# Performance work log

Measured on AMD Instinct MI355X. Metric: run time of the kernel, lower is better.

Reference implementation:

```python
import jax, jax.numpy as jnp
import numpy as np

D_MODEL = 512
NUM_HEADS = 8
D_FF = 2048
HEAD_DIM = D_MODEL // NUM_HEADS
EPS = 1e-8


def rmsnorm(x, scale):
    rms = jax.lax.rsqrt(jnp.mean(x * x, axis=-1, keepdims=True) + EPS)
    return scale * x * rms


def alibi_bias(seq_len, num_heads):
    # faithful to: 1.0 / (arange(1,H+1) * 2**arange(0,8)[:,None]).flatten()[:H]
    a = jnp.arange(1, num_heads + 1, dtype=jnp.float32)          # (H,)
    b = 2.0 ** jnp.arange(0, 8, dtype=jnp.float32)[:, None]       # (8,1)
    slopes = (1.0 / (a * b).reshape(-1))[:num_heads]               # (H,)
    pos = jnp.arange(seq_len)
    dist = jnp.abs(pos[:, None] - pos[None, :]).astype(jnp.float32)  # (S,S)
    return -slopes[:, None, None] * dist[None]                     # (H,S,S)


def setup_inputs() -> dict:
    key = jax.random.key(0)
    ks = jax.random.split(key, 12)
    s = 0.02
    return {
        "x": jax.random.normal(ks[0], (2, 2048, D_MODEL), dtype=jnp.float32),
        "norm1_scale": jnp.ones((D_MODEL,), jnp.float32),
        "norm2_scale": jnp.ones((D_MODEL,), jnp.float32),
        "in_proj_w": jax.random.normal(ks[1], (3 * D_MODEL, D_MODEL), jnp.float32) * s,
        "in_proj_b": jnp.zeros((3 * D_MODEL,), jnp.float32),
        "out_proj_w": jax.random.normal(ks[2], (D_MODEL, D_MODEL), jnp.float32) * s,
        "out_proj_b": jnp.zeros((D_MODEL,), jnp.float32),
        "w1": jax.random.normal(ks[3], (D_FF, D_MODEL), jnp.float32) * s,
        "b1": jnp.zeros((D_FF,), jnp.float32),
        "w2": jax.random.normal(ks[4], (D_MODEL, D_FF), jnp.float32) * s,
        "b2": jnp.zeros((D_MODEL,), jnp.float32),
    }


def reference(x, norm1_scale, norm2_scale, in_proj_w, in_proj_b,
              out_proj_w, out_proj_b, w1, b1, w2, b2):
    B, S, D = x.shape
    xn = rmsnorm(x, norm1_scale)
    qkv = xn @ in_proj_w.T + in_proj_b                      # (B,S,3D)
    q, k, v = jnp.split(qkv, 3, axis=-1)
    q = q.reshape(B, S, NUM_HEADS, HEAD_DIM)
    k = k.reshape(B, S, NUM_HEADS, HEAD_DIM)
    v = v.reshape(B, S, NUM_HEADS, HEAD_DIM)
    scale = 1.0 / jnp.sqrt(jnp.float32(HEAD_DIM))
    scores = jnp.einsum('bqhd,bkhd->bhqk', q, k) * scale    # (B,H,S,S)
    scores = scores + alibi_bias(S, NUM_HEADS)[None]
    attn = jax.nn.softmax(scores, axis=-1)
    ctx = jnp.einsum('bhqk,bkhd->bqhd', attn, v).reshape(B, S, D)
    attn_out = ctx @ out_proj_w.T + out_proj_b
    x = x + attn_out                                        # dropout is identity (eval)
    xn2 = rmsnorm(x, norm2_scale)
    h = jax.nn.gelu(xn2 @ w1.T + b1, approximate=False)
    mlp_out = h @ w2.T + b2
    return x + mlp_out
```

## Files before the change

kernel.cpp:

```cpp
#include <hip/hip_runtime.h>
#include <math.h>


typedef __bf16 bf16x8 __attribute__((ext_vector_type(8)));
typedef float  f32x4  __attribute__((ext_vector_type(4)));

#define TOKENS 4096
#define DMODEL 512
#define SEQ    2048
#define QSCALE 0.1803368801f

__device__ __forceinline__ void gl_lds16(const __bf16* g, __bf16* l) {
    __builtin_amdgcn_global_load_lds(
        (const __attribute__((address_space(1))) void*)g,
        (__attribute__((address_space(3))) void*)l, 16, 0, 0);
}

union PkU { unsigned u; __bf16 h[2]; };

__global__ void pre_kernel(const float* __restrict__ x, const float* __restrict__ n1s,
                           __bf16* __restrict__ xn1,
                           const float* __restrict__ w0, const float* __restrict__ w1,
                           const float* __restrict__ w2, const float* __restrict__ w3,
                           __bf16* __restrict__ d0, __bf16* __restrict__ d1,
                           __bf16* __restrict__ d2, __bf16* __restrict__ d3) {
    if (blockIdx.x < 1024) {
        int wave = threadIdx.x >> 6, lane = threadIdx.x & 63;
        int tok = blockIdx.x * 4 + wave;
        const float* row = x + (size_t)tok * DMODEL;
        float4 v0 = *(const float4*)&row[lane * 4];
        float4 v1 = *(const float4*)&row[256 + lane * 4];
        float ss = v0.x*v0.x + v0.y*v0.y + v0.z*v0.z + v0.w*v0.w
                 + v1.x*v1.x + v1.y*v1.y + v1.z*v1.z + v1.w*v1.w;
        #pragma unroll
        for (int off = 1; off < 64; off <<= 1) ss += __shfl_xor(ss, off);
        float r = rsqrtf(ss * (1.0f / DMODEL) + 1e-8f);
        __bf16* o = xn1 + (size_t)tok * DMODEL;
        o[lane*4 + 0] = (__bf16)(v0.x * r * n1s[lane*4 + 0]);
        o[lane*4 + 1] = (__bf16)(v0.y * r * n1s[lane*4 + 1]);
        o[lane*4 + 2] = (__bf16)(v0.z * r * n1s[lane*4 + 2]);
        o[lane*4 + 3] = (__bf16)(v0.w * r * n1s[lane*4 + 3]);
        o[256 + lane*4 + 0] = (__bf16)(v1.x * r * n1s[256 + lane*4 + 0]);
        o[256 + lane*4 + 1] = (__bf16)(v1.y * r * n1s[256 + lane*4 + 1]);
        o[256 + lane*4 + 2] = (__bf16)(v1.z * r * n1s[256 + lane*4 + 2]);
        o[256 + lane*4 + 3] = (__bf16)(v1.w * r * n1s[256 + lane*4 + 3]);
    } else {
        const int N0 = 1536 * 512, N1 = 512 * 512, N2 = 2048 * 512, N3 = 512 * 2048;
        int i4 = ((blockIdx.x - 1024) * 256 + threadIdx.x) * 4;
        const float* s; __bf16* d;
        if (i4 < N0)              { s = w0 + i4;  d = d0 + i4; }
        else if ((i4 -= N0) < N1) { s = w1 + i4;  d = d1 + i4; }
        else if ((i4 -= N1) < N2) { s = w2 + i4;  d = d2 + i4; }
        else if ((i4 -= N2) < N3) { s = w3 + i4;  d = d3 + i4; }
        else return;
        float4 v = *(const float4*)s;
        d[0] = (__bf16)v.x; d[1] = (__bf16)v.y; d[2] = (__bf16)v.z; d[3] = (__bf16)v.w;
    }
}

__global__ void rmsnorm_kernel(const float* __restrict__ x, const float* __restrict__ scale,
                               __bf16* __restrict__ out) {
    int wave = threadIdx.x >> 6, lane = threadIdx.x & 63;
    int tok = blockIdx.x * 4 + wave;
    const float* row = x + (size_t)tok * DMODEL;
    float4 v0 = *(const float4*)&row[lane * 4];
    float4 v1 = *(const float4*)&row[256 + lane * 4];
    float ss = v0.x*v0.x + v0.y*v0.y + v0.z*v0.z + v0.w*v0.w
             + v1.x*v1.x + v1.y*v1.y + v1.z*v1.z + v1.w*v1.w;
    #pragma unroll
    for (int off = 1; off < 64; off <<= 1) ss += __shfl_xor(ss, off);
    float r = rsqrtf(ss * (1.0f / DMODEL) + 1e-8f);
    __bf16* o = out + (size_t)tok * DMODEL;
    o[lane*4 + 0] = (__bf16)(v0.x * r * scale[lane*4 + 0]);
    o[lane*4 + 1] = (__bf16)(v0.y * r * scale[lane*4 + 1]);
    o[lane*4 + 2] = (__bf16)(v0.z * r * scale[lane*4 + 2]);
    o[lane*4 + 3] = (__bf16)(v0.w * r * scale[lane*4 + 3]);
    o[256 + lane*4 + 0] = (__bf16)(v1.x * r * scale[256 + lane*4 + 0]);
    o[256 + lane*4 + 1] = (__bf16)(v1.y * r * scale[256 + lane*4 + 1]);
    o[256 + lane*4 + 2] = (__bf16)(v1.z * r * scale[256 + lane*4 + 2]);
    o[256 + lane*4 + 3] = (__bf16)(v1.w * r * scale[256 + lane*4 + 3]);
}

template <int EPI, int TM, int KS = 1>
__global__ __launch_bounds__(256) void gemm_bt(
    const __bf16* __restrict__ A, const __bf16* __restrict__ W,
    const float* __restrict__ bias, const float* __restrict__ res,
    float* __restrict__ Cf, __bf16* __restrict__ Cb,
    __bf16* __restrict__ qb, __bf16* __restrict__ kb, __bf16* __restrict__ vtb,
    int M, int N, int K)
{
    constexpr int RI = TM / 32;
    __shared__ alignas(16) __bf16 As[2][TM * 32];
    __shared__ alignas(16) __bf16 Bs[2][128 * 32];
    const int tid = threadIdx.x;
    const int bm = blockIdx.x * TM;
    const int bn = blockIdx.y * 128;
    const int wave = tid >> 6, lane = tid & 63;
    const int wm = (wave & 1) * (TM / 2), wn = (wave >> 1) * 64;
    const int lrow = lane & 15;
    const int kq = (lane >> 4) * 8;

    f32x4 acc[RI][4] = {};

    const int Kc = K / KS;
    const int kbeg = (KS > 1) ? blockIdx.z * Kc : 0;

    for (int k0 = kbeg; k0 < kbeg + Kc; k0 += 64) {
        __syncthreads();
        #pragma unroll
        for (int i = 0; i < TM / 32; i++) {
            int tt = i * 256 + tid;
            int kh = tt / (TM * 4), rem = tt % (TM * 4);
            int mrow = rem >> 2, c8 = rem & 3;
            gl_lds16(&A[(size_t)(bm + mrow) * K + k0 + kh * 32 + c8 * 8],
                     (__bf16*)As + tt * 8);
        }
        #pragma unroll
        for (int i = 0; i < 4; i++) {
            int tt = i * 256 + tid;
            int kh = tt >> 9, rem = tt & 511;
            int nrow = rem >> 2, c8 = rem & 3;
            gl_lds16(&W[(size_t)(bn + nrow) * K + k0 + kh * 32 + c8 * 8],
                     (__bf16*)Bs + tt * 8);
        }
        __syncthreads();
        #pragma unroll
        for (int kh = 0; kh < 2; kh++) {
            bf16x8 af[RI], bfv[4];
            #pragma unroll
            for (int i = 0; i < RI; i++) af[i] = *(bf16x8*)&As[kh][(wm + i*16 + lrow)*32 + kq];
            #pragma unroll
            for (int j = 0; j < 4; j++) bfv[j] = *(bf16x8*)&Bs[kh][(wn + j*16 + lrow)*32 + kq];
            #pragma unroll
            for (int i = 0; i < RI; i++)
                #pragma unroll
                for (int j = 0; j < 4; j++)
                    acc[i][j] = __builtin_amdgcn_mfma_f32_16x16x32_bf16(af[i], bfv[j], acc[i][j], 0, 0, 0);
        }
    }

    const int crow0 = (lane >> 4) * 4;
    const int ccol = lane & 15;
    const int quad = lane >> 4;

    if (EPI == 4) {
        #pragma unroll
        for (int j = 0; j < 4; j++) {
            const int col = bn + wn + j * 16 + ccol;
            const float bv = bias[col];
            if (col < 512) {
                const int h = col >> 6, d = col & 63;
                #pragma unroll
                for (int i = 0; i < RI; i++) {
                    const int row0 = bm + wm + i * 16 + crow0;
                    const int b = row0 >> 11, s0 = row0 & 2047;
                    #pragma unroll
                    for (int r = 0; r < 4; r++)
                        qb[(((size_t)b*8 + h)*2048 + s0 + r)*64 + d] =
                            (__bf16)((acc[i][j][r] + bv) * QSCALE);
                }
            } else if (col < 1024) {
                const int h = (col - 512) >> 6, d = col & 63;
                #pragma unroll
                for (int i = 0; i < RI; i++) {
                    const int row0 = bm + wm + i * 16 + crow0;
                    const int b = row0 >> 11, s0 = row0 & 2047;
                    #pragma unroll
                    for (int r = 0; r < 4; r++)
                        kb[(((size_t)b*8 + h)*2048 + s0 + r)*64 + d] = (__bf16)(acc[i][j][r] + bv);
                }
            } else {
                const int h = (col - 1024) >> 6, d = col & 63;
                const int tok0 = bm + wm;
                const int b = tok0 >> 11, sbase = tok0 & 2047;
                unsigned* vrow = (unsigned*)vtb + (((size_t)b*8 + h)*64 + d) * 1024 + (sbase >> 1);
                #pragma unroll
                for (int ip = 0; ip < RI / 2; ip++) {
                    #pragma unroll
                    for (int r = 0; r < 4; r++) {
                        PkU pk;
                        pk.h[0] = (__bf16)(acc[2*ip][j][r] + bv);
                        pk.h[1] = (__bf16)(acc[2*ip+1][j][r] + bv);
                        vrow[ip * 16 + quad * 4 + r] = pk.u;
                    }
                }
            }
        }
    } else {
        #pragma unroll
        for (int i = 0; i < RI; i++) {
            const int row0 = bm + wm + i * 16 + crow0;
            #pragma unroll
            for (int j = 0; j < 4; j++) {
                const int col = bn + wn + j * 16 + ccol;
                if (EPI == 1) {
                    const float bv = bias[col];
                    #pragma unroll
                    for (int r = 0; r < 4; r++) {
                        const size_t idx = (size_t)(row0 + r) * N + col;
                        Cf[idx] = res[idx] + acc[i][j][r] + bv;
                    }
                } else if (EPI == 2) {
                    const float bv = bias[col];
                    #pragma unroll
                    for (int r = 0; r < 4; r++) {
                        float v = acc[i][j][r] + bv;
                        float u = v * (0.7978845608f + 0.0356774081f * v * v);
                        float t = exp2f(u * 2.8853900818f);
                        Cb[(size_t)(row0 + r) * N + col] = (__bf16)(v - v / (t + 1.0f));
                    }
                } else {
                    const size_t zoff = (size_t)blockIdx.z * M * N;
                    #pragma unroll
                    for (int r = 0; r < 4; r++)
                        Cf[zoff + (size_t)(row0 + r) * N + col] = acc[i][j][r];
                }
            }
        }
    }
}

__global__ __launch_bounds__(256) void attn_kernel(
    const __bf16* __restrict__ qb, const __bf16* __restrict__ kb,
    const __bf16* __restrict__ vtb, __bf16* __restrict__ ctx)
{
    const int id = blockIdx.x;
    const int qt = id >> 4;
    const int bh = (id & 15) ^ (7 * (id >> 8));
    const int h = bh & 7, b = bh >> 3;
    const int tid = threadIdx.x, wave = tid >> 6, lane = tid & 63;
    const int lrow = lane & 15, quad = lane >> 4;

    __shared__ alignas(16) __bf16 Ks[2][2][64 * 32];
    __shared__ alignas(16) __bf16 Vt[2][2][64 * 32];
    __shared__ alignas(16) unsigned Pt4[4][2][16][20];

    const float slope2 = -1.44269504f / (float)(h + 1);
    const int q0 = qt * 64;
    const int D = 16 * (h + 1) + 16;
    const int kt_lo = max(0, q0 - D) >> 6;
    const int kt_hi = min(SEQ - 1, q0 + 63 + D) >> 6;

    bf16x8 qf[2];
    #pragma unroll
    for (int dh = 0; dh < 2; dh++)
        qf[dh] = *(const bf16x8*)&qb[((size_t)bh*2048 + q0 + wave*16 + lrow)*64 + dh*32 + quad*8];

    bf16x8 ones;
    #pragma unroll
    for (int j = 0; j < 8; j++) ones[j] = (__bf16)1.0f;

    f32x4 O[4] = {};
    f32x4 lacc = {};

    auto stage = [&](int kt, int buf) {
        const int kbase = kt * 64;
        #pragma unroll
        for (int i = 0; i < 2; i++) {
            int tt = i * 256 + tid;
            int dh = tt >> 8, key = (tt & 255) >> 2, c8 = (tt & 3) * 8;
            gl_lds16(&kb[((size_t)bh*2048 + kbase + key)*64 + dh*32 + c8],
                     (__bf16*)Ks[buf] + tt * 8);
        }
        #pragma unroll
        for (int i = 0; i < 2; i++) {
            int tt = i * 256 + tid;
            int kh = tt >> 8, d = (tt & 255) >> 2, ck = (tt & 3) * 8;
            gl_lds16(&vtb[((size_t)bh*64 + d)*2048 + kbase + kh*32 + ck],
                     (__bf16*)Vt[buf] + tt * 8);
        }
    };

    stage(kt_lo, 0);

    for (int kt = kt_lo, buf = 0; kt <= kt_hi; kt++, buf ^= 1) {
        __syncthreads();
        if (kt < kt_hi) stage(kt + 1, buf ^ 1);

        bf16x8 kf[4][2];
        #pragma unroll
        for (int j = 0; j < 4; j++)
            #pragma unroll
            for (int dh = 0; dh < 2; dh++)
                kf[j][dh] = *(bf16x8*)&Ks[buf][dh][(j*16 + lrow)*32 + quad*8];

        f32x4 Sc[4] = {};
        #pragma unroll
        for (int dh = 0; dh < 2; dh++)
            #pragma unroll
            for (int j = 0; j < 4; j++)
                Sc[j] = __builtin_amdgcn_mfma_f32_16x16x32_bf16(qf[dh], kf[j][dh], Sc[j], 0, 0, 0);

        const float dbase = (float)(q0 + wave*16 + quad*4 - kt*64 - lrow);
        #pragma unroll
        for (int r = 0; r < 4; r++) {
            const float d0 = dbase + (float)r;
            #pragma unroll
            for (int jp = 0; jp < 2; jp++) {
                float v0 = fmaf(slope2, fabsf(d0 - (float)(jp*32)),      Sc[2*jp  ][r]);
                float v1 = fmaf(slope2, fabsf(d0 - (float)(jp*32 + 16)), Sc[2*jp+1][r]);
                PkU pk;
                pk.h[0] = (__bf16)exp2f(v0);
                pk.h[1] = (__bf16)exp2f(v1);
                Pt4[wave][jp][quad*4 + r][lrow] = pk.u;
            }
        }

        bf16x8 pf[2];
        #pragma unroll
        for (int kh = 0; kh < 2; kh++)
            pf[kh] = *(bf16x8*)&Pt4[wave][kh][lrow][quad*4];

        #pragma unroll
        for (int kh = 0; kh < 2; kh++)
            lacc = __builtin_amdgcn_mfma_f32_16x16x32_bf16(pf[kh], ones, lacc, 0, 0, 0);

        #pragma unroll
        for (int dt = 0; dt < 4; dt++) {
            #pragma unroll
            for (int kh = 0; kh < 2; kh++) {
                bf16x8 vf = *(bf16x8*)&Vt[buf][kh][(dt*16 + lrow)*32 + quad*8];
                O[dt] = __builtin_amdgcn_mfma_f32_16x16x32_bf16(pf[kh], vf, O[dt], 0, 0, 0);
            }
        }
    }

    #pragma unroll
    for (int dt = 0; dt < 4; dt++) {
        #pragma unroll
        for (int r = 0; r < 4; r++) {
            const int q = q0 + wave*16 + quad*4 + r;
            ctx[((size_t)(b * 2048 + q)) * DMODEL + h * 64 + dt*16 + lrow] =
                (__bf16)(O[dt][r] / lacc[r]);
        }
    }
}

__global__ void combine2_kernel(const float* __restrict__ p, const float* __restrict__ x1,
                                const float* __restrict__ b2, float* __restrict__ out) {
    const int i4 = (blockIdx.x * 256 + threadIdx.x) * 4;
    float4 a  = *(const float4*)&x1[i4];
    float4 b  = *(const float4*)&b2[i4 & 511];
    float4 c0 = *(const float4*)&p[i4];
    float4 c1 = *(const float4*)&p[(size_t)TOKENS * DMODEL + i4];
    float4 o;
    o.x = a.x + b.x + c0.x + c1.x;
    o.y = a.y + b.y + c0.y + c1.y;
    o.z = a.z + b.z + c0.z + c1.z;
    o.w = a.w + b.w + c0.w + c1.w;
    *(float4*)&out[i4] = o;
}

extern "C" void kernel_launch(void* const* d_in, const int* in_sizes, int n_in,
                              void* d_out, int out_size, void* d_ws, size_t ws_size,
                              hipStream_t stream) {
    const float* x    = (const float*)d_in[0];
    const float* n1s  = (const float*)d_in[1];
    const float* n2s  = (const float*)d_in[2];
    const float* wqkv = (const float*)d_in[3];
    const float* bqkv = (const float*)d_in[4];
    const float* wout = (const float*)d_in[5];
    const float* bout = (const float*)d_in[6];
    const float* w1   = (const float*)d_in[7];
    const float* b1   = (const float*)d_in[8];
    const float* w2   = (const float*)d_in[9];
    const float* b2   = (const float*)d_in[10];
    float* out = (float*)d_out;

    char* ws = (char*)d_ws;
    __bf16* xn1     = (__bf16*)ws; ws += (size_t)TOKENS * DMODEL * 2;
    __bf16* qbuf    = (__bf16*)ws; ws += (size_t)TOKENS * DMODEL * 2;
    __bf16* kbuf    = (__bf16*)ws; ws += (size_t)TOKENS * DMODEL * 2;
    __bf16* vtbuf   = (__bf16*)ws; ws += (size_t)TOKENS * DMODEL * 2;
    __bf16* wqkv_b  = (__bf16*)ws; ws += (size_t)1536 * DMODEL * 2;
    __bf16* wout_b  = (__bf16*)ws; ws += (size_t)DMODEL * DMODEL * 2;
    __bf16* w1_b    = (__bf16*)ws; ws += (size_t)2048 * DMODEL * 2;
    __bf16* w2_b    = (__bf16*)ws; ws += (size_t)DMODEL * 2048 * 2;
    __bf16* ctx     = (__bf16*)ws; ws += (size_t)TOKENS * DMODEL * 2;
    float*  x1      = (float*)ws;  ws += (size_t)TOKENS * DMODEL * 4;
    __bf16* xn2     = (__bf16*)ws; ws += (size_t)TOKENS * DMODEL * 2;
    __bf16* hbuf    = (__bf16*)ws; ws += (size_t)TOKENS * 2048 * 2;
    float*  mlp2p   = (float*)ws;  ws += (size_t)2 * TOKENS * DMODEL * 4;

    pre_kernel<<<dim3(4096), 256, 0, stream>>>(x, n1s, xn1,
        wqkv, wout, w1, w2, wqkv_b, wout_b, w1_b, w2_b);

    gemm_bt<4, 64><<<dim3(TOKENS / 64, 1536 / 128), 256, 0, stream>>>(
        xn1, wqkv_b, bqkv, nullptr, nullptr, nullptr, qbuf, kbuf, vtbuf,
        TOKENS, 1536, DMODEL);

    attn_kernel<<<dim3(512), 256, 0, stream>>>(qbuf, kbuf, vtbuf, ctx);

    gemm_bt<1, 32><<<dim3(TOKENS / 32, DMODEL / 128), 256, 0, stream>>>(
        ctx, wout_b, bout, x, x1, nullptr, nullptr, nullptr, nullptr,
        TOKENS, DMODEL, DMODEL);

    rmsnorm_kernel<<<dim3(TOKENS / 4), 256, 0, stream>>>(x1, n2s, xn2);

    gemm_bt<2, 32><<<dim3(TOKENS / 32, 2048 / 128), 256, 0, stream>>>(
        xn2, w1_b, b1, nullptr, nullptr, hbuf, nullptr, nullptr, nullptr,
        TOKENS, 2048, DMODEL);

    gemm_bt<6, 32, 2><<<dim3(TOKENS / 32, DMODEL / 128, 2), 256, 0, stream>>>(
        hbuf, w2_b, nullptr, nullptr, mlp2p, nullptr, nullptr, nullptr, nullptr,
        TOKENS, DMODEL, 2048);

    combine2_kernel<<<dim3(TOKENS * DMODEL / 4 / 256), 256, 0, stream>>>(
        mlp2p, x1, b2, out);
}
```

Baseline: 172.7 us.

## Fuse out-proj with residual and RMSNorm, atomically accumulate FFN2 into output

A new out-projection kernel computes full 512-wide rows per block, so it can add the residual, compute the second RMSNorm in its epilogue, and write both the normalized bf16 activations and the pre-initialised output (residual plus b2). The split-K FFN2 GEMM now atomically adds its partial sums straight into the output, which removes the separate rmsnorm and combine kernels and the fp32 partial buffers. The QKV GEMM also switches to a 64-wide N tile for more blocks. The costs are that each out-proj block reloads the whole weight matrix for only 16 rows, that atomics make the summation order nondeterministic, and that there is fp32 atomic contention.

```diff
diff --git a/kernel.cpp b/kernel.cpp
--- a/kernel.cpp
+++ b/kernel.cpp
@@ -58,49 +58,27 @@
     }
 }
 
-__global__ void rmsnorm_kernel(const float* __restrict__ x, const float* __restrict__ scale,
-                               __bf16* __restrict__ out) {
-    int wave = threadIdx.x >> 6, lane = threadIdx.x & 63;
-    int tok = blockIdx.x * 4 + wave;
-    const float* row = x + (size_t)tok * DMODEL;
-    float4 v0 = *(const float4*)&row[lane * 4];
-    float4 v1 = *(const float4*)&row[256 + lane * 4];
-    float ss = v0.x*v0.x + v0.y*v0.y + v0.z*v0.z + v0.w*v0.w
-             + v1.x*v1.x + v1.y*v1.y + v1.z*v1.z + v1.w*v1.w;
-    #pragma unroll
-    for (int off = 1; off < 64; off <<= 1) ss += __shfl_xor(ss, off);
-    float r = rsqrtf(ss * (1.0f / DMODEL) + 1e-8f);
-    __bf16* o = out + (size_t)tok * DMODEL;
-    o[lane*4 + 0] = (__bf16)(v0.x * r * scale[lane*4 + 0]);
-    o[lane*4 + 1] = (__bf16)(v0.y * r * scale[lane*4 + 1]);
-    o[lane*4 + 2] = (__bf16)(v0.z * r * scale[lane*4 + 2]);
-    o[lane*4 + 3] = (__bf16)(v0.w * r * scale[lane*4 + 3]);
-    o[256 + lane*4 + 0] = (__bf16)(v1.x * r * scale[256 + lane*4 + 0]);
-    o[256 + lane*4 + 1] = (__bf16)(v1.y * r * scale[256 + lane*4 + 1]);
-    o[256 + lane*4 + 2] = (__bf16)(v1.z * r * scale[256 + lane*4 + 2]);
-    o[256 + lane*4 + 3] = (__bf16)(v1.w * r * scale[256 + lane*4 + 3]);
-}
-
-template <int EPI, int TM, int KS = 1>
+template <int EPI, int TM, int TN, int KS = 1>
 __global__ __launch_bounds__(256) void gemm_bt(
     const __bf16* __restrict__ A, const __bf16* __restrict__ W,
-    const float* __restrict__ bias, const float* __restrict__ res,
+    const float* __restrict__ bias,
     float* __restrict__ Cf, __bf16* __restrict__ Cb,
     __bf16* __restrict__ qb, __bf16* __restrict__ kb, __bf16* __restrict__ vtb,
     int M, int N, int K)
 {
     constexpr int RI = TM / 32;
+    constexpr int NJ = TN / 32;
     __shared__ alignas(16) __bf16 As[2][TM * 32];
-    __shared__ alignas(16) __bf16 Bs[2][128 * 32];
+    __shared__ alignas(16) __bf16 Bs[2][TN * 32];
     const int tid = threadIdx.x;
     const int bm = blockIdx.x * TM;
-    const int bn = blockIdx.y * 128;
+    const int bn = blockIdx.y * TN;
     const int wave = tid >> 6, lane = tid & 63;
-    const int wm = (wave & 1) * (TM / 2), wn = (wave >> 1) * 64;
+    const int wm = (wave & 1) * (TM / 2), wn = (wave >> 1) * (TN / 2);
     const int lrow = lane & 15;
     const int kq = (lane >> 4) * 8;
 
-    f32x4 acc[RI][4] = {};
+    f32x4 acc[RI][NJ] = {};
 
     const int Kc = K / KS;
     const int kbeg = (KS > 1) ? blockIdx.z * Kc : 0;
@@ -116,9 +94,9 @@
                      (__bf16*)As + tt * 8);
         }
         #pragma unroll
-        for (int i = 0; i < 4; i++) {
+        for (int i = 0; i < TN / 32; i++) {
             int tt = i * 256 + tid;
-            int kh = tt >> 9, rem = tt & 511;
+            int kh = tt / (TN * 4), rem = tt % (TN * 4);
             int nrow = rem >> 2, c8 = rem & 3;
             gl_lds16(&W[(size_t)(bn + nrow) * K + k0 + kh * 32 + c8 * 8],
                      (__bf16*)Bs + tt * 8);
@@ -126,15 +104,15 @@
         __syncthreads();
         #pragma unroll
         for (int kh = 0; kh < 2; kh++) {
-            bf16x8 af[RI], bfv[4];
+            bf16x8 af[RI], bfv[NJ];
             #pragma unroll
             for (int i = 0; i < RI; i++) af[i] = *(bf16x8*)&As[kh][(wm + i*16 + lrow)*32 + kq];
             #pragma unroll
-            for (int j = 0; j < 4; j++) bfv[j] = *(bf16x8*)&Bs[kh][(wn + j*16 + lrow)*32 + kq];
+            for (int j = 0; j < NJ; j++) bfv[j] = *(bf16x8*)&Bs[kh][(wn + j*16 + lrow)*32 + kq];
             #pragma unroll
             for (int i = 0; i < RI; i++)
                 #pragma unroll
-                for (int j = 0; j < 4; j++)
+                for (int j = 0; j < NJ; j++)
                     acc[i][j] = __builtin_amdgcn_mfma_f32_16x16x32_bf16(af[i], bfv[j], acc[i][j], 0, 0, 0);
         }
     }
@@ -145,7 +123,7 @@
 
     if (EPI == 4) {
         #pragma unroll
-        for (int j = 0; j < 4; j++) {
+        for (int j = 0; j < NJ; j++) {
             const int col = bn + wn + j * 16 + ccol;
             const float bv = bias[col];
             if (col < 512) {
@@ -191,16 +169,9 @@
         for (int i = 0; i < RI; i++) {
             const int row0 = bm + wm + i * 16 + crow0;
             #pragma unroll
-            for (int j = 0; j < 4; j++) {
+            for (int j = 0; j < NJ; j++) {
                 const int col = bn + wn + j * 16 + ccol;
-                if (EPI == 1) {
-                    const float bv = bias[col];
-                    #pragma unroll
-                    for (int r = 0; r < 4; r++) {
-                        const size_t idx = (size_t)(row0 + r) * N + col;
-                        Cf[idx] = res[idx] + acc[i][j][r] + bv;
-                    }
-                } else if (EPI == 2) {
+                if (EPI == 2) {
                     const float bv = bias[col];
                     #pragma unroll
                     for (int r = 0; r < 4; r++) {
@@ -210,12 +181,104 @@
                         Cb[(size_t)(row0 + r) * N + col] = (__bf16)(v - v / (t + 1.0f));
                     }
                 } else {
-                    const size_t zoff = (size_t)blockIdx.z * M * N;
                     #pragma unroll
                     for (int r = 0; r < 4; r++)
-                        Cf[zoff + (size_t)(row0 + r) * N + col] = acc[i][j][r];
+                        unsafeAtomicAdd(&Cf[(size_t)(row0 + r) * N + col], acc[i][j][r]);
                 }
             }
+        }
+    }
+}
+
+__global__ __launch_bounds__(256) void outproj_kernel(
+    const __bf16* __restrict__ ctx, const __bf16* __restrict__ W,
+    const float* __restrict__ bout, const float* __restrict__ x,
+    const float* __restrict__ n2s, const float* __restrict__ b2,
+    __bf16* __restrict__ xn2, float* __restrict__ out)
+{
+    __shared__ alignas(16) __bf16 As[2][16 * 32];
+    __shared__ alignas(16) __bf16 Bs[2][512 * 32];
+    __shared__ float rsum[4][16];
+    const int tid = threadIdx.x;
+    const int bm = blockIdx.x * 16;
+    const int wave = tid >> 6, lane = tid & 63;
+    const int wn = wave * 128;
+    const int lrow = lane & 15;
+    const int kq = (lane >> 4) * 8;
+
+    f32x4 acc[8] = {};
+
+    for (int k0 = 0; k0 < 512; k0 += 64) {
+        __syncthreads();
+        if (tid < 128) {
+            int kh = tid >> 6, rem = tid & 63;
+            int mrow = rem >> 2, c8 = rem & 3;
+            gl_lds16(&ctx[(size_t)(bm + mrow) * 512 + k0 + kh * 32 + c8 * 8],
+                     (__bf16*)As + tid * 8);
+        }
+        #pragma unroll
+        for (int i = 0; i < 16; i++) {
+            int tt = i * 256 + tid;
+            int kh = tt >> 11, rem = tt & 2047;
+            int nrow = rem >> 2, c8 = rem & 3;
+            gl_lds16(&W[(size_t)nrow * 512 + k0 + kh * 32 + c8 * 8],
+                     (__bf16*)Bs + tt * 8);
+        }
+        __syncthreads();
+        #pragma unroll
+        for (int kh = 0; kh < 2; kh++) {
+            bf16x8 af = *(bf16x8*)&As[kh][lrow * 32 + kq];
+            #pragma unroll
+            for (int j = 0; j < 8; j++) {
+                bf16x8 bf = *(bf16x8*)&Bs[kh][(wn + j*16 + lrow)*32 + kq];
+                acc[j] = __builtin_amdgcn_mfma_f32_16x16x32_bf16(af, bf, acc[j], 0, 0, 0);
+            }
+        }
+    }
+
+    const int quad = lane >> 4;
+    const int ccol = lane & 15;
+    float xv[8][4];
+    float ss[4] = {};
+    #pragma unroll
+    for (int j = 0; j < 8; j++) {
+        const int col = wn + j * 16 + ccol;
+        const float bv = bout[col];
+        #pragma unroll
+        for (int r = 0; r < 4; r++) {
+            const int row = bm + quad * 4 + r;
+            float v = x[(size_t)row * 512 + col] + acc[j][r] + bv;
+            xv[j][r] = v;
+            ss[r] += v * v;
+        }
+    }
+    #pragma unroll
+    for (int r = 0; r < 4; r++) {
+        #pragma unroll
+        for (int off = 1; off < 16; off <<= 1)
+            ss[r] += __shfl_xor(ss[r], off);
+    }
+    if (ccol == 0) {
+        #pragma unroll
+        for (int r = 0; r < 4; r++) rsum[wave][quad * 4 + r] = ss[r];
+    }
+    __syncthreads();
+    float rms[4];
+    #pragma unroll
+    for (int r = 0; r < 4; r++) {
+        float tot = rsum[0][quad*4 + r] + rsum[1][quad*4 + r]
+                  + rsum[2][quad*4 + r] + rsum[3][quad*4 + r];
+        rms[r] = rsqrtf(tot * (1.0f / 512.0f) + 1e-8f);
+    }
+    #pragma unroll
+    for (int j = 0; j < 8; j++) {
+        const int col = wn + j * 16 + ccol;
+        const float sc = n2s[col], bb = b2[col];
+        #pragma unroll
+        for (int r = 0; r < 4; r++) {
+            const int row = bm + quad * 4 + r;
+            xn2[(size_t)row * 512 + col] = (__bf16)(xv[j][r] * rms[r] * sc);
+            out[(size_t)row * 512 + col] = xv[j][r] + bb;
         }
     }
 }
@@ -334,21 +397,6 @@
                 (__bf16)(O[dt][r] / lacc[r]);
         }
     }
-}
-
-__global__ void combine2_kernel(const float* __restrict__ p, const float* __restrict__ x1,
-                                const float* __restrict__ b2, float* __restrict__ out) {
-    const int i4 = (blockIdx.x * 256 + threadIdx.x) * 4;
-    float4 a  = *(const float4*)&x1[i4];
-    float4 b  = *(const float4*)&b2[i4 & 511];
-    float4 c0 = *(const float4*)&p[i4];
-    float4 c1 = *(const float4*)&p[(size_t)TOKENS * DMODEL + i4];
-    float4 o;
-    o.x = a.x + b.x + c0.x + c1.x;
-    o.y = a.y + b.y + c0.y + c1.y;
-    o.z = a.z + b.z + c0.z + c1.z;
-    o.w = a.w + b.w + c0.w + c1.w;
-    *(float4*)&out[i4] = o;
 }
 
 extern "C" void kernel_launch(void* const* d_in, const int* in_sizes, int n_in,
@@ -377,34 +425,26 @@
     __bf16* w1_b    = (__bf16*)ws; ws += (size_t)2048 * DMODEL * 2;
     __bf16* w2_b    = (__bf16*)ws; ws += (size_t)DMODEL * 2048 * 2;
     __bf16* ctx     = (__bf16*)ws; ws += (size_t)TOKENS * DMODEL * 2;
-    float*  x1      = (float*)ws;  ws += (size_t)TOKENS * DMODEL * 4;
     __bf16* xn2     = (__bf16*)ws; ws += (size_t)TOKENS * DMODEL * 2;
     __bf16* hbuf    = (__bf16*)ws; ws += (size_t)TOKENS * 2048 * 2;
-    float*  mlp2p   = (float*)ws;  ws += (size_t)2 * TOKENS * DMODEL * 4;
 
     pre_kernel<<<dim3(4096), 256, 0, stream>>>(x, n1s, xn1,
         wqkv, wout, w1, w2, wqkv_b, wout_b, w1_b, w2_b);
 
-    gemm_bt<4, 64><<<dim3(TOKENS / 64, 1536 / 128), 256, 0, stream>>>(
-        xn1, wqkv_b, bqkv, nullptr, nullptr, nullptr, qbuf, kbuf, vtbuf,
+    gemm_bt<4, 64, 64><<<dim3(TOKENS / 64, 1536 / 64), 256, 0, stream>>>(
+        xn1, wqkv_b, bqkv, nullptr, nullptr, qbuf, kbuf, vtbuf,
         TOKENS, 1536, DMODEL);
 
     attn_kernel<<<dim3(512), 256, 0, stream>>>(qbuf, kbuf, vtbuf, ctx);
 
-    gemm_bt<1, 32><<<dim3(TOKENS / 32, DMODEL / 128), 256, 0, stream>>>(
-        ctx, wout_b, bout, x, x1, nullptr, nullptr, nullptr, nullptr,
-        TOKENS, DMODEL, DMODEL);
-
-    rmsnorm_kernel<<<dim3(TOKENS / 4), 256, 0, stream>>>(x1, n2s, xn2);
-
-    gemm_bt<2, 32><<<dim3(TOKENS / 32, 2048 / 128), 256, 0, stream>>>(
-        xn2, w1_b, b1, nullptr, nullptr, hbuf, nullptr, nullptr, nullptr,
+    outproj_kernel<<<dim3(TOKENS / 16), 256, 0, stream>>>(
+        ctx, wout_b, bout, x, n2s, b2, xn2, out);
+
+    gemm_bt<2, 32, 128><<<dim3(TOKENS / 32, 2048 / 128), 256, 0, stream>>>(
+        xn2, w1_b, b1, nullptr, hbuf, nullptr, nullptr, nullptr,
         TOKENS, 2048, DMODEL);
 
-    gemm_bt<6, 32, 2><<<dim3(TOKENS / 32, DMODEL / 128, 2), 256, 0, stream>>>(
-        hbuf, w2_b, nullptr, nullptr, mlp2p, nullptr, nullptr, nullptr, nullptr,
+    gemm_bt<5, 32, 128, 2><<<dim3(TOKENS / 32, DMODEL / 128, 2), 256, 0, stream>>>(
+        hbuf, w2_b, nullptr, out, nullptr, nullptr, nullptr, nullptr,
         TOKENS, DMODEL, 2048);
-
-    combine2_kernel<<<dim3(TOKENS * DMODEL / 4 / 256), 256, 0, stream>>>(
-        mlp2p, x1, b2, out);
-}
+}
```

Result: slower. 179.4 us (+3.9%).

## Replace split-K partial buffer and combine kernel with atomic accumulation into output

Applied to the files above, without the earlier changes.

The second-norm kernel now also writes x1 + b2 into the output. The split-K MLP-down GEMM then atomically adds its partial results into that output, so the partial buffer and the separate combine kernel are removed. The MLP-up GEMM also moves from 32-row to 64-row tiles. This saves one launch and the write and re-read of two full fp32 partial arrays, at the cost of float atomics, whose summation order is non-deterministic.

```diff
diff --git a/kernel.cpp b/kernel.cpp
--- a/kernel.cpp
+++ b/kernel.cpp
@@ -58,11 +58,12 @@
     }
 }
 
-__global__ void rmsnorm_kernel(const float* __restrict__ x, const float* __restrict__ scale,
-                               __bf16* __restrict__ out) {
+__global__ void rmsnorm2_kernel(const float* __restrict__ x1, const float* __restrict__ scale,
+                                const float* __restrict__ b2,
+                                __bf16* __restrict__ xn2, float* __restrict__ outInit) {
     int wave = threadIdx.x >> 6, lane = threadIdx.x & 63;
     int tok = blockIdx.x * 4 + wave;
-    const float* row = x + (size_t)tok * DMODEL;
+    const float* row = x1 + (size_t)tok * DMODEL;
     float4 v0 = *(const float4*)&row[lane * 4];
     float4 v1 = *(const float4*)&row[256 + lane * 4];
     float ss = v0.x*v0.x + v0.y*v0.y + v0.z*v0.z + v0.w*v0.w
@@ -70,7 +71,7 @@
     #pragma unroll
     for (int off = 1; off < 64; off <<= 1) ss += __shfl_xor(ss, off);
     float r = rsqrtf(ss * (1.0f / DMODEL) + 1e-8f);
-    __bf16* o = out + (size_t)tok * DMODEL;
+    __bf16* o = xn2 + (size_t)tok * DMODEL;
     o[lane*4 + 0] = (__bf16)(v0.x * r * scale[lane*4 + 0]);
     o[lane*4 + 1] = (__bf16)(v0.y * r * scale[lane*4 + 1]);
     o[lane*4 + 2] = (__bf16)(v0.z * r * scale[lane*4 + 2]);
@@ -79,6 +80,12 @@
     o[256 + lane*4 + 1] = (__bf16)(v1.y * r * scale[256 + lane*4 + 1]);
     o[256 + lane*4 + 2] = (__bf16)(v1.z * r * scale[256 + lane*4 + 2]);
     o[256 + lane*4 + 3] = (__bf16)(v1.w * r * scale[256 + lane*4 + 3]);
+    float4 b0 = *(const float4*)&b2[lane * 4];
+    float4 b1v = *(const float4*)&b2[256 + lane * 4];
+    float4 w0 = make_float4(v0.x + b0.x, v0.y + b0.y, v0.z + b0.z, v0.w + b0.w);
+    float4 w1 = make_float4(v1.x + b1v.x, v1.y + b1v.y, v1.z + b1v.z, v1.w + b1v.w);
+    *(float4*)&outInit[(size_t)tok * DMODEL + lane * 4] = w0;
+    *(float4*)&outInit[(size_t)tok * DMODEL + 256 + lane * 4] = w1;
 }
 
 template <int EPI, int TM, int KS = 1>
@@ -210,10 +217,9 @@
                         Cb[(size_t)(row0 + r) * N + col] = (__bf16)(v - v / (t + 1.0f));
                     }
                 } else {
-                    const size_t zoff = (size_t)blockIdx.z * M * N;
                     #pragma unroll
                     for (int r = 0; r < 4; r++)
-                        Cf[zoff + (size_t)(row0 + r) * N + col] = acc[i][j][r];
+                        unsafeAtomicAdd(&Cf[(size_t)(row0 + r) * N + col], acc[i][j][r]);
                 }
             }
         }
@@ -334,21 +340,6 @@
                 (__bf16)(O[dt][r] / lacc[r]);
         }
     }
-}
-
-__global__ void combine2_kernel(const float* __restrict__ p, const float* __restrict__ x1,
-                                const float* __restrict__ b2, float* __restrict__ out) {
-    const int i4 = (blockIdx.x * 256 + threadIdx.x) * 4;
-    float4 a  = *(const float4*)&x1[i4];
-    float4 b  = *(const float4*)&b2[i4 & 511];
-    float4 c0 = *(const float4*)&p[i4];
-    float4 c1 = *(const float4*)&p[(size_t)TOKENS * DMODEL + i4];
-    float4 o;
-    o.x = a.x + b.x + c0.x + c1.x;
-    o.y = a.y + b.y + c0.y + c1.y;
-    o.z = a.z + b.z + c0.z + c1.z;
-    o.w = a.w + b.w + c0.w + c1.w;
-    *(float4*)&out[i4] = o;
 }
 
 extern "C" void kernel_launch(void* const* d_in, const int* in_sizes, int n_in,
@@ -380,7 +371,6 @@
     float*  x1      = (float*)ws;  ws += (size_t)TOKENS * DMODEL * 4;
     __bf16* xn2     = (__bf16*)ws; ws += (size_t)TOKENS * DMODEL * 2;
     __bf16* hbuf    = (__bf16*)ws; ws += (size_t)TOKENS * 2048 * 2;
-    float*  mlp2p   = (float*)ws;  ws += (size_t)2 * TOKENS * DMODEL * 4;
 
     pre_kernel<<<dim3(4096), 256, 0, stream>>>(x, n1s, xn1,
         wqkv, wout, w1, w2, wqkv_b, wout_b, w1_b, w2_b);
@@ -395,16 +385,13 @@
         ctx, wout_b, bout, x, x1, nullptr, nullptr, nullptr, nullptr,
         TOKENS, DMODEL, DMODEL);
 
-    rmsnorm_kernel<<<dim3(TOKENS / 4), 256, 0, stream>>>(x1, n2s, xn2);
-
-    gemm_bt<2, 32><<<dim3(TOKENS / 32, 2048 / 128), 256, 0, stream>>>(
+    rmsnorm2_kernel<<<dim3(TOKENS / 4), 256, 0, stream>>>(x1, n2s, b2, xn2, out);
+
+    gemm_bt<2, 64><<<dim3(TOKENS / 64, 2048 / 128), 256, 0, stream>>>(
         xn2, w1_b, b1, nullptr, nullptr, hbuf, nullptr, nullptr, nullptr,
         TOKENS, 2048, DMODEL);
 
-    gemm_bt<6, 32, 2><<<dim3(TOKENS / 32, DMODEL / 128, 2), 256, 0, stream>>>(
-        hbuf, w2_b, nullptr, nullptr, mlp2p, nullptr, nullptr, nullptr, nullptr,
+    gemm_bt<5, 32, 2><<<dim3(TOKENS / 32, DMODEL / 128, 2), 256, 0, stream>>>(
+        hbuf, w2_b, nullptr, nullptr, out, nullptr, nullptr, nullptr, nullptr,
         TOKENS, DMODEL, 2048);
-
-    combine2_kernel<<<dim3(TOKENS * DMODEL / 4 / 256), 256, 0, stream>>>(
-        mlp2p, x1, b2, out);
-}
+}
```

New measurement: 171.0 us. Within noise of the previous version (-1.0%).
